# Optimization experiments

Hardware: AMD Instinct MI355X
Metric: run time of the kernel (lower is better)

Reference implementation:

```python
import jax, jax.numpy as jnp
import numpy as np

B, A, QS, KS = 8, 6, 32, 1024   # batch, agents, query_size, key_size
C, H, W_ = 256, 64, 64          # value feature-map dims


def setup_inputs() -> dict:
    key = jax.random.key(0)
    k1, k2, k3, k4 = jax.random.split(key, 4)
    qu = jax.random.normal(k1, (B, A, QS), dtype=jnp.float32)
    k = jax.random.normal(k2, (B, A, KS), dtype=jnp.float32)
    v = jax.random.normal(k3, (B, A, C, H, W_), dtype=jnp.float32)
    W = jax.random.normal(k4, (KS, QS), dtype=jnp.float32) * (1.0 / np.sqrt(QS))
    b = jnp.zeros((KS,), dtype=jnp.float32)
    return {"qu": qu, "k": k, "v": v, "W": W, "b": b}


def reference(qu, k, v, W, b):
    # Linear projection of query messages: [B, Q, query_size] -> [B, Q, key_size]
    query = qu @ W.T + b
    # Attention scores: bmm(k, query^T) -> [B, K, Q]
    attn = jnp.einsum('bkd,bqd->bkq', k, query)
    # Softmax over the key (agent) dim, matching nn.Softmax(dim=1)
    attn_sm = jax.nn.softmax(attn, axis=1)
    # Fused weighted combine over keys (replaces 6D expand-mul-sum):
    # sum_k attn[b,k,q] * v[b,k,c,h,w] -> [B, Q, C, H, W]
    out = jnp.einsum('bkq,bkchw->bqchw', attn_sm, v)
    return (out, attn_sm)
```

## Files before the change

### kernel.cpp

```cpp
#include <hip/hip_runtime.h>
#include <hip/hip_bf16.h>

constexpr int B  = 8;
constexpr int A  = 6;
constexpr int QS = 32;
constexpr int KS = 1024;
constexpr int C  = 256;
constexpr int H  = 64;
constexpr int W_ = 64;
constexpr long CHW  = (long)C * H * W_;
constexpr long CHW4 = CHW / 4;
constexpr int  BLOCKS_PER_B = (int)(CHW4 / 256);

__global__ __launch_bounds__(256) void attn_kernel(
    const float* __restrict__ qu,
    const float* __restrict__ kmat,
    const float* __restrict__ Wm,
    const float* __restrict__ bias,
    float* __restrict__ attn_out)
{
    __shared__ float s_qu[A * QS];
    __shared__ float s_query[A][KS];
    __shared__ float s_attn[A][A];

    const int b   = blockIdx.x;
    const int tid = threadIdx.x;

    for (int i = tid; i < A * QS; i += 256) s_qu[i] = qu[b * A * QS + i];
    __syncthreads();

    for (int i = tid; i < A * KS; i += 256) {
        const int q = i >> 10;
        const int d = i & (KS - 1);
        float acc = bias[d];
        const float* wrow = Wm + d * QS;
        const float* qrow = s_qu + q * QS;
        #pragma unroll
        for (int s = 0; s < QS; ++s) acc += qrow[s] * wrow[s];
        s_query[q][d] = acc;
    }
    __syncthreads();

    const int wave = tid >> 6;
    const int lane = tid & 63;
    for (int p = wave; p < A * A; p += 4) {
        const int kk = p / A;
        const int q  = p % A;
        const float* krow = kmat + ((long)b * A + kk) * KS;
        float partial = 0.f;
        for (int d = lane; d < KS; d += 64) partial += krow[d] * s_query[q][d];
        #pragma unroll
        for (int off = 32; off > 0; off >>= 1)
            partial += __shfl_down(partial, off, 64);
        if (lane == 0) s_attn[kk][q] = partial;
    }
    __syncthreads();

    if (tid < A) {
        const int q = tid;
        float m = s_attn[0][q];
        #pragma unroll
        for (int kk = 1; kk < A; ++kk) m = fmaxf(m, s_attn[kk][q]);
        float e[A];
        float sum = 0.f;
        #pragma unroll
        for (int kk = 0; kk < A; ++kk) { e[kk] = expf(s_attn[kk][q] - m); sum += e[kk]; }
        const float inv = 1.f / sum;
        #pragma unroll
        for (int kk = 0; kk < A; ++kk)
            attn_out[b * A * A + kk * A + q] = e[kk] * inv;
    }
}

__global__ __launch_bounds__(256) void combine_kernel(
    const float* __restrict__ v,
    const float* __restrict__ attn,
    float* __restrict__ out)
{
    __shared__ float s_a[A * A];

    const int b   = blockIdx.x >> 10;
    const int blk = blockIdx.x & (BLOCKS_PER_B - 1);

    if (threadIdx.x < A * A) s_a[threadIdx.x] = attn[b * A * A + threadIdx.x];
    __syncthreads();

    const long i4   = (long)blk * 256 + threadIdx.x;
    const long base = (long)b * A * CHW4 + i4;
    const float4* vb = reinterpret_cast<const float4*>(v)   + base;
    float4*       ob = reinterpret_cast<float4*>(out)       + base;

    float4 vv[A];
    #pragma unroll
    for (int kk = 0; kk < A; ++kk) vv[kk] = vb[(long)kk * CHW4];

    #pragma unroll
    for (int q = 0; q < A; ++q) {
        float4 acc = make_float4(0.f, 0.f, 0.f, 0.f);
        #pragma unroll
        for (int kk = 0; kk < A; ++kk) {
            const float a = s_a[kk * A + q];
            acc.x += a * vv[kk].x;
            acc.y += a * vv[kk].y;
            acc.z += a * vv[kk].z;
            acc.w += a * vv[kk].w;
        }
        ob[(long)q * CHW4] = acc;
    }
}

extern "C" void kernel_launch(void* const* d_in, const int* in_sizes, int n_in,
                              void* d_out, int out_size, void* d_ws, size_t ws_size,
                              hipStream_t stream) {
    const float* qu   = (const float*)d_in[0];
    const float* kmat = (const float*)d_in[1];
    const float* v    = (const float*)d_in[2];
    const float* Wm   = (const float*)d_in[3];
    const float* bias = (const float*)d_in[4];

    float* out      = (float*)d_out;
    float* attn_out = out + (long)B * A * CHW;

    attn_kernel<<<B, 256, 0, stream>>>(qu, kmat, Wm, bias, attn_out);
    combine_kernel<<<B * BLOCKS_PER_B, 256, 0, stream>>>(v, attn_out, out);
}
```

Baseline: 407.7 us.

## Stage W tiles in LDS for projection and use nontemporal loads/stores in combine

The attention kernel now loads W in coalesced 256-row chunks into padded shared memory, and each thread computes all six query rows for one key dimension, reusing each W value instead of reading strided rows from global memory. The combine kernel reads the attention weights straight into registers instead of staging them through shared memory with a barrier. It also uses nontemporal loads and stores for the streaming v and output traffic to avoid polluting caches. The combine kernel is a bandwidth-bound stream, so the nontemporal hints may have little effect. The attention kernel runs on only eight blocks and is a small share of total time.

```diff
diff --git a/kernel.cpp b/kernel.cpp
--- a/kernel.cpp
+++ b/kernel.cpp
@@ -12,6 +12,8 @@
 constexpr long CHW4 = CHW / 4;
 constexpr int  BLOCKS_PER_B = (int)(CHW4 / 256);
 
+typedef float f32x4 __attribute__((ext_vector_type(4)));
+
 __global__ __launch_bounds__(256) void attn_kernel(
     const float* __restrict__ qu,
     const float* __restrict__ kmat,
@@ -19,27 +21,47 @@
     const float* __restrict__ bias,
     float* __restrict__ attn_out)
 {
-    __shared__ float s_qu[A * QS];
+    __shared__ float s_qu[A][QS];
+    __shared__ float s_w[256][QS + 1];
     __shared__ float s_query[A][KS];
     __shared__ float s_attn[A][A];
 
     const int b   = blockIdx.x;
     const int tid = threadIdx.x;
 
-    for (int i = tid; i < A * QS; i += 256) s_qu[i] = qu[b * A * QS + i];
+    for (int i = tid; i < A * QS; i += 256) s_qu[i / QS][i % QS] = qu[b * A * QS + i];
     __syncthreads();
 
-    for (int i = tid; i < A * KS; i += 256) {
-        const int q = i >> 10;
-        const int d = i & (KS - 1);
-        float acc = bias[d];
-        const float* wrow = Wm + d * QS;
-        const float* qrow = s_qu + q * QS;
+    for (int chunk = 0; chunk < KS / 256; ++chunk) {
+        const f32x4* wsrc = reinterpret_cast<const f32x4*>(Wm + (long)chunk * 256 * QS);
         #pragma unroll
-        for (int s = 0; s < QS; ++s) acc += qrow[s] * wrow[s];
-        s_query[q][d] = acc;
+        for (int j = 0; j < 8; ++j) {
+            const int f4  = j * 256 + tid;
+            const f32x4 w4 = wsrc[f4];
+            const int row = f4 >> 3;
+            const int col = (f4 & 7) * 4;
+            s_w[row][col + 0] = w4.x;
+            s_w[row][col + 1] = w4.y;
+            s_w[row][col + 2] = w4.z;
+            s_w[row][col + 3] = w4.w;
+        }
+        __syncthreads();
+
+        const int d  = chunk * 256 + tid;
+        const float bd = bias[d];
+        float acc[A];
+        #pragma unroll
+        for (int q = 0; q < A; ++q) acc[q] = bd;
+        #pragma unroll
+        for (int s = 0; s < QS; ++s) {
+            const float w = s_w[tid][s];
+            #pragma unroll
+            for (int q = 0; q < A; ++q) acc[q] += w * s_qu[q][s];
+        }
+        #pragma unroll
+        for (int q = 0; q < A; ++q) s_query[q][d] = acc[q];
+        __syncthreads();
     }
-    __syncthreads();
 
     const int wave = tid >> 6;
     const int lane = tid & 63;
@@ -77,35 +99,31 @@
     const float* __restrict__ attn,
     float* __restrict__ out)
 {
-    __shared__ float s_a[A * A];
-
     const int b   = blockIdx.x >> 10;
     const int blk = blockIdx.x & (BLOCKS_PER_B - 1);
 
-    if (threadIdx.x < A * A) s_a[threadIdx.x] = attn[b * A * A + threadIdx.x];
-    __syncthreads();
+    float a[A * A];
+    const float* __restrict__ ab = attn + b * A * A;
+    #pragma unroll
+    for (int i = 0; i < A * A; ++i) a[i] = ab[i];
 
     const long i4   = (long)blk * 256 + threadIdx.x;
     const long base = (long)b * A * CHW4 + i4;
-    const float4* vb = reinterpret_cast<const float4*>(v)   + base;
-    float4*       ob = reinterpret_cast<float4*>(out)       + base;
+    const f32x4* __restrict__ vb = reinterpret_cast<const f32x4*>(v)   + base;
+    f32x4*       __restrict__ ob = reinterpret_cast<f32x4*>(out)       + base;
 
-    float4 vv[A];
+    f32x4 vv[A];
     #pragma unroll
-    for (int kk = 0; kk < A; ++kk) vv[kk] = vb[(long)kk * CHW4];
+    for (int kk = 0; kk < A; ++kk)
+        vv[kk] = __builtin_nontemporal_load(vb + (long)kk * CHW4);
 
     #pragma unroll
     for (int q = 0; q < A; ++q) {
-        float4 acc = make_float4(0.f, 0.f, 0.f, 0.f);
+        f32x4 acc = (f32x4){0.f, 0.f, 0.f, 0.f};
         #pragma unroll
-        for (int kk = 0; kk < A; ++kk) {
-            const float a = s_a[kk * A + q];
-            acc.x += a * vv[kk].x;
-            acc.y += a * vv[kk].y;
-            acc.z += a * vv[kk].z;
-            acc.w += a * vv[kk].w;
-        }
-        ob[(long)q * CHW4] = acc;
+        for (int kk = 0; kk < A; ++kk)
+            acc += a[kk * A + q] * vv[kk];
+        __builtin_nontemporal_store(acc, ob + (long)q * CHW4);
     }
 }
 
```

Result: faster. 382.5 us (-6.2%).
